# Kernel tuning notes

Hardware: AMD Instinct MI355X
Metric: run time of the kernel (lower is better)

## Reference

```python
import jax, jax.numpy as jnp
import numpy as np

UNITS = 1024
D_MODEL = 1024
H = 16
DK = 64
DV = 64
M = 128
B = 4
S = 1024


def setup_inputs() -> dict:
    key = jax.random.key(0)
    ks = jax.random.split(key, 12)
    s = 1.0 / np.sqrt(D_MODEL)
    inp = {
        "queries": jax.random.normal(ks[0], (B, S, D_MODEL), jnp.float32),
        "keys": jax.random.normal(ks[1], (B, S, D_MODEL), jnp.float32),
        "values": jax.random.normal(ks[2], (B, S, D_MODEL), jnp.float32),
        "Wq": jax.random.normal(ks[3], (D_MODEL, H * DK), jnp.float32) * s,
        "bq": jnp.zeros((H * DK,), jnp.float32),
        "Wk": jax.random.normal(ks[4], (D_MODEL, H * DK), jnp.float32) * s,
        "bk": jnp.zeros((H * DK,), jnp.float32),
        "Wv": jax.random.normal(ks[5], (D_MODEL, H * DV), jnp.float32) * s,
        "bv": jnp.zeros((H * DV,), jnp.float32),
        "Wo": jax.random.normal(ks[6], (H * DV, UNITS), jnp.float32) * (1.0 / np.sqrt(H * DV)),
        "bo": jnp.zeros((UNITS,), jnp.float32),
        "mk": jax.random.normal(ks[7], (1, M, H * DK), jnp.float32) * 0.1,
        "mv": jax.random.normal(ks[8], (1, M, H * DV), jnp.float32) * 0.1,
        "h": H,
    }
    return inp


def reference(queries, keys, values, Wq, bq, Wk, bk, Wv, bv, Wo, bo, mk, mv, h):
    Bq, Sq, _ = queries.shape
    m = mk.shape[1]
    dk = Wk.shape[1] // h
    dv = Wv.shape[1] // h
    scale_m = jnp.sqrt(jnp.asarray(m, queries.dtype))

    # Q projection: [B, h, Sq, dk]
    q = (queries @ Wq + bq).reshape(Bq, Sq, h, dk).transpose(0, 2, 1, 3)

    # K/V projections with m learned memory slots concatenated on the seq axis
    k_flat = jnp.concatenate(
        [keys @ Wk + bk, scale_m * jnp.broadcast_to(mk, (Bq, m, h * dk))], axis=1
    )  # [B, Sk+m, h*dk]
    v_flat = jnp.concatenate(
        [values @ Wv + bv, scale_m * jnp.broadcast_to(mv, (Bq, m, h * dv))], axis=1
    )  # [B, Sk+m, h*dv]
    Skm = k_flat.shape[1]
    k = k_flat.reshape(Bq, Skm, h, dk).transpose(0, 2, 1, 3)  # [B, h, Sk+m, dk]
    v = v_flat.reshape(Bq, Skm, h, dv).transpose(0, 2, 1, 3)  # [B, h, Sk+m, dv]

    # Scaled dot-product attention over sequence + memory slots
    scores = jnp.einsum("bhqd,bhkd->bhqk", q, k) / jnp.sqrt(jnp.asarray(dk, q.dtype))
    attn = jax.nn.softmax(scores, axis=-1)  # [B, h, Sq, Sk+m]
    out = jnp.einsum("bhqk,bhkd->bhqd", attn, v)  # [B, h, Sq, dv]
    out = out.transpose(0, 2, 1, 3).reshape(Bq, Sq, h * dv)
    return out @ Wo + bo
```

## Files before the change

### kernel.cpp

```cpp
#include <hip/hip_runtime.h>

typedef __attribute__((ext_vector_type(8))) __bf16 bf16x8;
typedef __attribute__((ext_vector_type(4))) float f32x4;

#define DEVINL __device__ __forceinline__

constexpr int BZ = 4;
constexpr int SEQ = 1024;
constexpr int DMODEL = 1024;
constexpr int NH = 16;
constexpr int HD = 64;
constexpr int MSLOT = 128;
constexpr int NT = BZ * SEQ;
constexpr int SKM = SEQ + MSLOT;
constexpr int VT_LD = BZ * SKM;
constexpr float SCALE_M = 11.313708498984761f;
constexpr float SCEXP = 0.18033688011112042f;
constexpr size_t OF_QIN  = 0;
constexpr size_t OF_KIN  = OF_QIN  + (size_t)NT * DMODEL;
constexpr size_t OF_VIN  = OF_KIN  + (size_t)NT * DMODEL;
constexpr size_t OF_WQT  = OF_VIN  + (size_t)NT * DMODEL;
constexpr size_t OF_WKT  = OF_WQT  + (size_t)DMODEL * DMODEL;
constexpr size_t OF_WVT  = OF_WKT  + (size_t)DMODEL * DMODEL;
constexpr size_t OF_WOT  = OF_WVT  + (size_t)DMODEL * DMODEL;
constexpr size_t OF_QB   = OF_WOT  + (size_t)DMODEL * DMODEL;
constexpr size_t OF_KPR  = OF_QB   + (size_t)NT * DMODEL;
constexpr size_t OF_KMEM = OF_KPR  + (size_t)NT * DMODEL;
constexpr size_t OF_VTG  = OF_KMEM + (size_t)MSLOT * DMODEL;
constexpr size_t OF_AOUT = OF_VTG  + (size_t)DMODEL * VT_LD;

DEVINL unsigned short f2bf(float f) {
  union { float f; unsigned u; } v; v.f = f;
  unsigned r = v.u + 0x7FFF + ((v.u >> 16) & 1);
  return (unsigned short)(r >> 16);
}

#if __has_builtin(__builtin_amdgcn_cvt_pk_bf16_f32)
DEVINL unsigned pack2(float a, float b) {
  auto t = __builtin_amdgcn_cvt_pk_bf16_f32(a, b);
  unsigned r; __builtin_memcpy(&r, &t, 4); return r;
}
#else
DEVINL unsigned pack2(float a, float b) {
  return (unsigned)f2bf(a) | ((unsigned)f2bf(b) << 16);
}
#endif

#if __has_builtin(__builtin_amdgcn_exp2f)
DEVINL float fast_exp2(float x) { return __builtin_amdgcn_exp2f(x); }
#else
DEVINL float fast_exp2(float x) { return exp2f(x); }
#endif

DEVINL f32x4 mfma16(bf16x8 a, bf16x8 b, f32x4 c) {
  return __builtin_amdgcn_mfma_f32_16x16x32_bf16(a, b, c, 0, 0, 0);
}

DEVINL void gload16(const unsigned short* gp, unsigned short* lp) {
  __builtin_amdgcn_global_load_lds(
      (const __attribute__((address_space(1))) unsigned int*)(const void*)gp,
      (__attribute__((address_space(3))) unsigned int*)(void*)lp, 16, 0, 0);
}


__global__ __launch_bounds__(256) void cvt3_bf16(const float* __restrict__ q,
                                                 const float* __restrict__ k,
                                                 const float* __restrict__ v,
                                                 unsigned short* __restrict__ dq,
                                                 unsigned short* __restrict__ dk,
                                                 unsigned short* __restrict__ dv) {
  const float* src = (blockIdx.y == 0) ? q : (blockIdx.y == 1) ? k : v;
  unsigned short* dst = (blockIdx.y == 0) ? dq : (blockIdx.y == 1) ? dk : dv;
  int i = (blockIdx.x * 256 + threadIdx.x) * 8;
  float4 v0 = *(const float4*)(src + i);
  float4 v1 = *(const float4*)(src + i + 4);
  union { unsigned u2[4]; uint4 v; } o;
  o.u2[0] = pack2(v0.x, v0.y); o.u2[1] = pack2(v0.z, v0.w);
  o.u2[2] = pack2(v1.x, v1.y); o.u2[3] = pack2(v1.z, v1.w);
  *(uint4*)(dst + i) = o.v;
}

__global__ __launch_bounds__(256) void transpose_cvt4(
    const float* __restrict__ s0, const float* __restrict__ s1,
    const float* __restrict__ s2, const float* __restrict__ s3,
    unsigned short* __restrict__ d0, unsigned short* __restrict__ d1,
    unsigned short* __restrict__ d2, unsigned short* __restrict__ d3) {
  const float* src = (blockIdx.z == 0) ? s0 : (blockIdx.z == 1) ? s1 : (blockIdx.z == 2) ? s2 : s3;
  unsigned short* dst = (blockIdx.z == 0) ? d0 : (blockIdx.z == 1) ? d1 : (blockIdx.z == 2) ? d2 : d3;
  __shared__ float t[32][65];
  const int tid = threadIdx.x;
  const int n0 = blockIdx.x * 32, k0 = blockIdx.y * 64;
  {
    int c = tid & 31, rg = tid >> 5;
#pragma unroll
    for (int rr = 0; rr < 8; ++rr)
      t[c][rg * 8 + rr] = src[(size_t)(k0 + rg * 8 + rr) * DMODEL + n0 + c];
  }
  __syncthreads();
  {
    int n = tid >> 3, ck = tid & 7;
    union { unsigned short u[8]; uint4 v; } o;
#pragma unroll
    for (int j = 0; j < 8; ++j) o.u[j] = f2bf(t[n][ck * 8 + j]);
    *(uint4*)(dst + (size_t)(n0 + n) * DMODEL + k0 + ck * 8) = o.v;
  }
}

__global__ __launch_bounds__(256) void kmem_cvt(const float* __restrict__ mk,
                                                unsigned short* __restrict__ dst) {
  int i = blockIdx.x * 256 + threadIdx.x;
  dst[i] = f2bf(mk[i] * SCALE_M);
}

__global__ __launch_bounds__(256) void vmem_transpose(const float* __restrict__ mv,
                                                      unsigned short* __restrict__ VtG) {
  __shared__ float t[32][33];
  const int tx = threadIdx.x, ty = threadIdx.y;
  const int j0 = blockIdx.x * 32, c0 = blockIdx.y * 32;
#pragma unroll
  for (int r = 0; r < 4; ++r)
    t[ty + r * 8][tx] = mv[(size_t)(j0 + ty + r * 8) * DMODEL + c0 + tx];
  __syncthreads();
#pragma unroll
  for (int r = 0; r < 4; ++r) {
    int c = c0 + ty + r * 8;
    unsigned short v = f2bf(t[tx][ty + r * 8] * SCALE_M);
#pragma unroll
    for (int bb = 0; bb < BZ; ++bb)
      VtG[(size_t)c * VT_LD + bb * SKM + SEQ + j0 + tx] = v;
  }
}


DEVINL void gemm_stage(const unsigned short* big, const unsigned short* sm,
                       unsigned short* B0, unsigned short* B1,
                       unsigned short* S0, unsigned short* S1,
                       int k0, int tid) {
#pragma unroll
  for (int hb = 0; hb < 2; ++hb) {
    unsigned short* bl = hb ? B1 : B0;
#pragma unroll
    for (int gi = 0; gi < 2; ++gi) {
      int g = gi * 256 + tid;
      int row = g >> 2, slot = g & 3;
      gload16(big + (size_t)row * DMODEL + k0 + hb * 32 + slot * 8, bl + g * 8);
    }
    unsigned short* sl = hb ? S1 : S0;
    int row = tid >> 2, slot = tid & 3;
    gload16(sm + (size_t)row * DMODEL + k0 + hb * 32 + slot * 8, sl + tid * 8);
  }
}

DEVINL void gemm_compute(const unsigned short* B0, const unsigned short* B1,
                         const unsigned short* S0, const unsigned short* S1,
                         int wr, int wc, int quad, int l16, f32x4 acc[4][2]) {
#pragma unroll
  for (int hb = 0; hb < 2; ++hb) {
    const unsigned short* bl = hb ? B1 : B0;
    const unsigned short* sl = hb ? S1 : S0;
    bf16x8 af[4], bfr[2];
#pragma unroll
    for (int rb = 0; rb < 4; ++rb)
      af[rb] = *(const bf16x8*)(bl + (wr * 64 + rb * 16 + l16) * 32 + quad * 8);
#pragma unroll
    for (int cb = 0; cb < 2; ++cb)
      bfr[cb] = *(const bf16x8*)(sl + (wc * 32 + cb * 16 + l16) * 32 + quad * 8);
#pragma unroll
    for (int rb = 0; rb < 4; ++rb)
#pragma unroll
      for (int cb = 0; cb < 2; ++cb)
        acc[rb][cb] = mfma16(af[rb], bfr[cb], acc[rb][cb]);
  }
}

__global__ __launch_bounds__(256) void proj_qkv(
    const unsigned short* __restrict__ Qin, const unsigned short* __restrict__ Kin,
    const unsigned short* __restrict__ Vin, const unsigned short* __restrict__ Wqt,
    const unsigned short* __restrict__ Wkt, const unsigned short* __restrict__ Wvt,
    const float* __restrict__ bq, const float* __restrict__ bk,
    const float* __restrict__ bv, unsigned short* __restrict__ Qbp,
    unsigned short* __restrict__ Kprp, unsigned short* __restrict__ VtG) {
  __shared__ unsigned short Big0[128 * 32], Big1[128 * 32];
  __shared__ unsigned short Sm0[64 * 32], Sm1[64 * 32];
  const int tid = threadIdx.x;
  const int pid = blockIdx.x >> 9;
  const int idx = blockIdx.x & 511;
  const int w = tid >> 6, lane = tid & 63, quad = lane >> 4, l16 = lane & 15;
  const int wr = w >> 1, wc = w & 1;
  f32x4 acc[4][2] = {};

  if (pid < 2) {
    const unsigned short* A  = pid ? Kin : Qin;
    const unsigned short* Wt = pid ? Wkt : Wqt;
    const float* bias        = pid ? bk : bq;
    unsigned short* out      = pid ? Kprp : Qbp;
    const int n0 = (idx & 15) * 64, m0 = (idx >> 4) * 128;
    const unsigned short* big = A + (size_t)m0 * DMODEL;
    const unsigned short* sm  = Wt + (size_t)n0 * DMODEL;
    for (int kt = 0; kt < 16; ++kt) {
      gemm_stage(big, sm, Big0, Big1, Sm0, Sm1, kt * 64, tid);
      __syncthreads();
      gemm_compute(Big0, Big1, Sm0, Sm1, wr, wc, quad, l16, acc);
      __syncthreads();
    }
#pragma unroll
    for (int rb = 0; rb < 4; ++rb)
#pragma unroll
      for (int cb = 0; cb < 2; ++cb)
#pragma unroll
        for (int r = 0; r < 4; ++r) {
          int row = m0 + wr * 64 + rb * 16 + quad * 4 + r;
          int col = n0 + wc * 32 + cb * 16 + l16;
          out[(size_t)row * DMODEL + col] = f2bf(acc[rb][cb][r] + bias[col]);
        }
  } else {
    const int t0 = (idx & 63) * 64, n0 = (idx >> 6) * 128;
    const unsigned short* big = Wvt + (size_t)n0 * DMODEL;
    const unsigned short* sm  = Vin + (size_t)t0 * DMODEL;
    for (int kt = 0; kt < 16; ++kt) {
      gemm_stage(big, sm, Big0, Big1, Sm0, Sm1, kt * 64, tid);
      __syncthreads();
      gemm_compute(Big0, Big1, Sm0, Sm1, wr, wc, quad, l16, acc);
      __syncthreads();
    }
#pragma unroll
    for (int rb = 0; rb < 4; ++rb)
#pragma unroll
      for (int cb = 0; cb < 2; ++cb)
#pragma unroll
        for (int r = 0; r < 4; ++r) {
          int n = n0 + wr * 64 + rb * 16 + quad * 4 + r;
          int tok = t0 + wc * 32 + cb * 16 + l16;
          int col = tok + (tok >> 10) * MSLOT;
          VtG[(size_t)n * VT_LD + col] = f2bf(acc[rb][cb][r] + bv[n]);
        }
  }
}

__global__ __launch_bounds__(256) void gemm_out(const unsigned short* __restrict__ A,
                                                const unsigned short* __restrict__ Wt,
                                                const float* __restrict__ bias,
                                                float* __restrict__ Cout) {
  __shared__ unsigned short Big0[128 * 32], Big1[128 * 32];
  __shared__ unsigned short Sm0[64 * 32], Sm1[64 * 32];
  const int tid = threadIdx.x;
  const int m0 = blockIdx.y * 128, n0 = blockIdx.x * 64;
  const int w = tid >> 6, lane = tid & 63, quad = lane >> 4, l16 = lane & 15;
  const int wr = w >> 1, wc = w & 1;
  f32x4 acc[4][2] = {};
  const unsigned short* big = A + (size_t)m0 * DMODEL;
  const unsigned short* sm  = Wt + (size_t)n0 * DMODEL;
  for (int kt = 0; kt < 16; ++kt) {
    gemm_stage(big, sm, Big0, Big1, Sm0, Sm1, kt * 64, tid);
    __syncthreads();
    gemm_compute(Big0, Big1, Sm0, Sm1, wr, wc, quad, l16, acc);
    __syncthreads();
  }
#pragma unroll
  for (int rb = 0; rb < 4; ++rb)
#pragma unroll
    for (int cb = 0; cb < 2; ++cb)
#pragma unroll
      for (int r = 0; r < 4; ++r) {
        int row = m0 + wr * 64 + rb * 16 + quad * 4 + r;
        int col = n0 + wc * 32 + cb * 16 + l16;
        Cout[(size_t)row * DMODEL + col] = acc[rb][cb][r] + bias[col];
      }
}

__global__ __launch_bounds__(256) void attn_kernel(const unsigned short* __restrict__ Qb,
                                                   const unsigned short* __restrict__ Kproj,
                                                   const unsigned short* __restrict__ Kmem,
                                                   const unsigned short* __restrict__ VtG,
                                                   unsigned short* __restrict__ Aout) {
  __shared__ unsigned short Ks[64 * 72];
  __shared__ unsigned short Vs[64 * 72];
  __shared__ unsigned short Pl[4 * 16 * 72];
  const int tid = threadIdx.x;
  const int bh = blockIdx.x & 63, qb = blockIdx.x >> 6;
  const int b = bh & 3, h = bh >> 2;
  const int w = tid >> 6, lane = tid & 63, quad = lane >> 4, l16 = lane & 15;
  const int token0 = b * SEQ + qb * 64 + w * 16;
  unsigned short* Pw = Pl + w * 16 * 72;

  const int g0 = tid, g1 = tid + 256;
  const int row0 = g0 >> 3, slot0 = g0 & 7;
  const int row1 = g1 >> 3, slot1 = g1 & 7;

  auto kbase = [&](int tile) -> const unsigned short* {
    return (tile < 16) ? Kproj + (size_t)(b * SEQ + tile * 64) * DMODEL + h * HD
                       : Kmem + (size_t)((tile - 16) * 64) * DMODEL + h * HD;
  };
  auto vbase = [&](int tile) -> const unsigned short* {
    int c0 = (tile < 16) ? b * SKM + tile * 64 : b * SKM + SEQ + (tile - 16) * 64;
    return VtG + (size_t)(h * HD) * VT_LD + c0;
  };

  bf16x8 qf[2];
#pragma unroll
  for (int t = 0; t < 2; ++t)
    qf[t] = *(const bf16x8*)(Qb + (size_t)(token0 + l16) * DMODEL + h * HD + t * 32 + quad * 8);

  f32x4 O[4] = {};
  float lsum = 0.0f;

  uint4 kr0, kr1, vr0, vr1;
  {
    const unsigned short* kp = kbase(0);
    const unsigned short* vp = vbase(0);
    kr0 = *(const uint4*)(kp + (size_t)row0 * DMODEL + slot0 * 8);
    kr1 = *(const uint4*)(kp + (size_t)row1 * DMODEL + slot1 * 8);
    vr0 = *(const uint4*)(vp + (size_t)row0 * VT_LD + slot0 * 8);
    vr1 = *(const uint4*)(vp + (size_t)row1 * VT_LD + slot1 * 8);
  }

  for (int tile = 0; tile < 18; ++tile) {
    *(uint4*)(Ks + row0 * 72 + slot0 * 8) = kr0;
    *(uint4*)(Ks + row1 * 72 + slot1 * 8) = kr1;
    *(uint4*)(Vs + row0 * 72 + slot0 * 8) = vr0;
    *(uint4*)(Vs + row1 * 72 + slot1 * 8) = vr1;
    __syncthreads();
    if (tile < 17) {
      const unsigned short* kp = kbase(tile + 1);
      const unsigned short* vp = vbase(tile + 1);
      kr0 = *(const uint4*)(kp + (size_t)row0 * DMODEL + slot0 * 8);
      kr1 = *(const uint4*)(kp + (size_t)row1 * DMODEL + slot1 * 8);
      vr0 = *(const uint4*)(vp + (size_t)row0 * VT_LD + slot0 * 8);
      vr1 = *(const uint4*)(vp + (size_t)row1 * VT_LD + slot1 * 8);
    }

    f32x4 sc[4] = {};
#pragma unroll
    for (int c = 0; c < 4; ++c)
#pragma unroll
      for (int t = 0; t < 2; ++t) {
        bf16x8 kb = *(const bf16x8*)(Ks + (c * 16 + l16) * 72 + t * 32 + quad * 8);
        sc[c] = mfma16(kb, qf[t], sc[c]);
      }

#pragma unroll
    for (int c = 0; c < 4; ++c) {
      float p0 = fast_exp2(sc[c][0] * SCEXP);
      float p1 = fast_exp2(sc[c][1] * SCEXP);
      float p2 = fast_exp2(sc[c][2] * SCEXP);
      float p3 = fast_exp2(sc[c][3] * SCEXP);
      lsum += (p0 + p1) + (p2 + p3);
      union { unsigned u[2]; } pk;
      pk.u[0] = pack2(p0, p1);
      pk.u[1] = pack2(p2, p3);
      *(uint2*)(Pw + l16 * 72 + c * 16 + quad * 4) = *(uint2*)pk.u;
    }
    __builtin_amdgcn_wave_barrier();

#pragma unroll
    for (int t2 = 0; t2 < 2; ++t2) {
      bf16x8 pa = *(const bf16x8*)(Pw + l16 * 72 + t2 * 32 + quad * 8);
#pragma unroll
      for (int c2 = 0; c2 < 4; ++c2) {
        bf16x8 vb = *(const bf16x8*)(Vs + (c2 * 16 + l16) * 72 + t2 * 32 + quad * 8);
        O[c2] = mfma16(pa, vb, O[c2]);
      }
    }
    __syncthreads();
  }

  lsum += __shfl_xor(lsum, 16);
  lsum += __shfl_xor(lsum, 32);
#pragma unroll
  for (int r = 0; r < 4; ++r) {
    float lv = __shfl(lsum, quad * 4 + r, 16);
    float inv = 1.0f / lv;
#pragma unroll
    for (int c2 = 0; c2 < 4; ++c2)
      Aout[(size_t)(token0 + quad * 4 + r) * DMODEL + h * HD + c2 * 16 + l16] =
          f2bf(O[c2][r] * inv);
  }
}

extern "C" void kernel_launch(void* const* d_in, const int* in_sizes, int n_in,
                              void* d_out, int out_size, void* d_ws, size_t ws_size,
                              hipStream_t stream) {
  const float* queries = (const float*)d_in[0];
  const float* keys    = (const float*)d_in[1];
  const float* values  = (const float*)d_in[2];
  const float* Wq = (const float*)d_in[3];
  const float* bq = (const float*)d_in[4];
  const float* Wk = (const float*)d_in[5];
  const float* bk = (const float*)d_in[6];
  const float* Wv = (const float*)d_in[7];
  const float* bv = (const float*)d_in[8];
  const float* Wo = (const float*)d_in[9];
  const float* bo = (const float*)d_in[10];
  const float* mk = (const float*)d_in[11];
  const float* mv = (const float*)d_in[12];

  unsigned short* ws = (unsigned short*)d_ws;
  unsigned short* Qin  = ws + OF_QIN;
  unsigned short* Kin  = ws + OF_KIN;
  unsigned short* Vin  = ws + OF_VIN;
  unsigned short* Wqt  = ws + OF_WQT;
  unsigned short* Wkt  = ws + OF_WKT;
  unsigned short* Wvt  = ws + OF_WVT;
  unsigned short* Wot  = ws + OF_WOT;
  unsigned short* Qbp  = ws + OF_QB;
  unsigned short* Kprp = ws + OF_KPR;
  unsigned short* Kmm  = ws + OF_KMEM;
  unsigned short* VtGp = ws + OF_VTG;
  unsigned short* Aoutp = ws + OF_AOUT;

  cvt3_bf16<<<dim3(2048, 3), 256, 0, stream>>>(queries, keys, values, Qin, Kin, Vin);

  transpose_cvt4<<<dim3(32, 16, 4), 256, 0, stream>>>(Wq, Wk, Wv, Wo, Wqt, Wkt, Wvt, Wot);

  kmem_cvt<<<(MSLOT * DMODEL) / 256, 256, 0, stream>>>(mk, Kmm);
  vmem_transpose<<<dim3(MSLOT / 32, DMODEL / 32), dim3(32, 8), 0, stream>>>(mv, VtGp);

  proj_qkv<<<1536, 256, 0, stream>>>(Qin, Kin, Vin, Wqt, Wkt, Wvt, bq, bk, bv,
                                     Qbp, Kprp, VtGp);

  attn_kernel<<<1024, 256, 0, stream>>>(Qbp, Kprp, Kmm, VtGp, Aoutp);

  gemm_out<<<dim3(16, 32), 256, 0, stream>>>(Aoutp, Wot, bo, (float*)d_out);
}
```

Measured before the change: 228.9 us.

## Enlarge GEMM tiles to 128x128 and process 32 queries per wave in attention

The projection and output GEMMs move from 128x64 tiles with a 64-wide k step to 128x128 tiles with a 32-wide k step. Each wave now holds a 4x4 accumulator block, so every loaded tile feeds more MFMAs and global traffic per FLOP drops. The attention kernel has each wave handle two 16-query groups, so each staged K/V tile in shared memory is reused for 128 queries per block. The launch grids are halved to match. The trade-offs are higher register use, fewer blocks to fill the CUs, and twice as many k-loop barriers in the GEMMs.

```diff
diff --git a/kernel.cpp b/kernel.cpp
--- a/kernel.cpp
+++ b/kernel.cpp
@@ -132,45 +132,31 @@
 }
 
 
-DEVINL void gemm_stage(const unsigned short* big, const unsigned short* sm,
-                       unsigned short* B0, unsigned short* B1,
-                       unsigned short* S0, unsigned short* S1,
-                       int k0, int tid) {
-#pragma unroll
-  for (int hb = 0; hb < 2; ++hb) {
-    unsigned short* bl = hb ? B1 : B0;
-#pragma unroll
-    for (int gi = 0; gi < 2; ++gi) {
-      int g = gi * 256 + tid;
-      int row = g >> 2, slot = g & 3;
-      gload16(big + (size_t)row * DMODEL + k0 + hb * 32 + slot * 8, bl + g * 8);
-    }
-    unsigned short* sl = hb ? S1 : S0;
-    int row = tid >> 2, slot = tid & 3;
-    gload16(sm + (size_t)row * DMODEL + k0 + hb * 32 + slot * 8, sl + tid * 8);
-  }
-}
-
-DEVINL void gemm_compute(const unsigned short* B0, const unsigned short* B1,
-                         const unsigned short* S0, const unsigned short* S1,
-                         int wr, int wc, int quad, int l16, f32x4 acc[4][2]) {
-#pragma unroll
-  for (int hb = 0; hb < 2; ++hb) {
-    const unsigned short* bl = hb ? B1 : B0;
-    const unsigned short* sl = hb ? S1 : S0;
-    bf16x8 af[4], bfr[2];
-#pragma unroll
-    for (int rb = 0; rb < 4; ++rb)
-      af[rb] = *(const bf16x8*)(bl + (wr * 64 + rb * 16 + l16) * 32 + quad * 8);
-#pragma unroll
-    for (int cb = 0; cb < 2; ++cb)
-      bfr[cb] = *(const bf16x8*)(sl + (wc * 32 + cb * 16 + l16) * 32 + quad * 8);
-#pragma unroll
-    for (int rb = 0; rb < 4; ++rb)
-#pragma unroll
-      for (int cb = 0; cb < 2; ++cb)
-        acc[rb][cb] = mfma16(af[rb], bfr[cb], acc[rb][cb]);
-  }
+DEVINL void g128_stage(const unsigned short* rA, const unsigned short* cB,
+                       unsigned short* As, unsigned short* Bs, int k0, int tid) {
+#pragma unroll
+  for (int gi = 0; gi < 2; ++gi) {
+    int g = gi * 256 + tid;
+    int row = g >> 2, slot = g & 3;
+    gload16(rA + (size_t)row * DMODEL + k0 + slot * 8, As + g * 8);
+    gload16(cB + (size_t)row * DMODEL + k0 + slot * 8, Bs + g * 8);
+  }
+}
+
+DEVINL void g128_compute(const unsigned short* As, const unsigned short* Bs,
+                         int wr, int wc, int quad, int l16, f32x4 acc[4][4]) {
+  bf16x8 af[4], bfr[4];
+#pragma unroll
+  for (int rb = 0; rb < 4; ++rb)
+    af[rb] = *(const bf16x8*)(As + (wr * 64 + rb * 16 + l16) * 32 + quad * 8);
+#pragma unroll
+  for (int cb = 0; cb < 4; ++cb)
+    bfr[cb] = *(const bf16x8*)(Bs + (wc * 64 + cb * 16 + l16) * 32 + quad * 8);
+#pragma unroll
+  for (int rb = 0; rb < 4; ++rb)
+#pragma unroll
+    for (int cb = 0; cb < 4; ++cb)
+      acc[rb][cb] = mfma16(af[rb], bfr[cb], acc[rb][cb]);
 }
 
 __global__ __launch_bounds__(256) void proj_qkv(
@@ -180,57 +166,58 @@
     const float* __restrict__ bq, const float* __restrict__ bk,
     const float* __restrict__ bv, unsigned short* __restrict__ Qbp,
     unsigned short* __restrict__ Kprp, unsigned short* __restrict__ VtG) {
-  __shared__ unsigned short Big0[128 * 32], Big1[128 * 32];
-  __shared__ unsigned short Sm0[64 * 32], Sm1[64 * 32];
+  __shared__ unsigned short As[128 * 32];
+  __shared__ unsigned short Bs[128 * 32];
   const int tid = threadIdx.x;
-  const int pid = blockIdx.x >> 9;
-  const int idx = blockIdx.x & 511;
+  const int pid = blockIdx.x >> 8;
+  const int idx = blockIdx.x & 255;
   const int w = tid >> 6, lane = tid & 63, quad = lane >> 4, l16 = lane & 15;
   const int wr = w >> 1, wc = w & 1;
-  f32x4 acc[4][2] = {};
+
+  const unsigned short *rA, *cB;
+  int m0, n0;
+  if (pid == 0) {
+    m0 = (idx >> 3) * 128; n0 = (idx & 7) * 128;
+    rA = Qin + (size_t)m0 * DMODEL; cB = Wqt + (size_t)n0 * DMODEL;
+  } else if (pid == 1) {
+    m0 = (idx >> 3) * 128; n0 = (idx & 7) * 128;
+    rA = Kin + (size_t)m0 * DMODEL; cB = Wkt + (size_t)n0 * DMODEL;
+  } else {
+    m0 = (idx & 7) * 128;
+    n0 = (idx >> 3) * 128;
+    rA = Wvt + (size_t)m0 * DMODEL; cB = Vin + (size_t)n0 * DMODEL;
+  }
+
+  f32x4 acc[4][4] = {};
+  for (int kt = 0; kt < 32; ++kt) {
+    g128_stage(rA, cB, As, Bs, kt * 32, tid);
+    __syncthreads();
+    g128_compute(As, Bs, wr, wc, quad, l16, acc);
+    __syncthreads();
+  }
 
   if (pid < 2) {
-    const unsigned short* A  = pid ? Kin : Qin;
-    const unsigned short* Wt = pid ? Wkt : Wqt;
-    const float* bias        = pid ? bk : bq;
-    unsigned short* out      = pid ? Kprp : Qbp;
-    const int n0 = (idx & 15) * 64, m0 = (idx >> 4) * 128;
-    const unsigned short* big = A + (size_t)m0 * DMODEL;
-    const unsigned short* sm  = Wt + (size_t)n0 * DMODEL;
-    for (int kt = 0; kt < 16; ++kt) {
-      gemm_stage(big, sm, Big0, Big1, Sm0, Sm1, kt * 64, tid);
-      __syncthreads();
-      gemm_compute(Big0, Big1, Sm0, Sm1, wr, wc, quad, l16, acc);
-      __syncthreads();
-    }
+    const float* bias = pid ? bk : bq;
+    unsigned short* out = pid ? Kprp : Qbp;
 #pragma unroll
     for (int rb = 0; rb < 4; ++rb)
 #pragma unroll
-      for (int cb = 0; cb < 2; ++cb)
+      for (int cb = 0; cb < 4; ++cb)
 #pragma unroll
         for (int r = 0; r < 4; ++r) {
           int row = m0 + wr * 64 + rb * 16 + quad * 4 + r;
-          int col = n0 + wc * 32 + cb * 16 + l16;
+          int col = n0 + wc * 64 + cb * 16 + l16;
           out[(size_t)row * DMODEL + col] = f2bf(acc[rb][cb][r] + bias[col]);
         }
   } else {
-    const int t0 = (idx & 63) * 64, n0 = (idx >> 6) * 128;
-    const unsigned short* big = Wvt + (size_t)n0 * DMODEL;
-    const unsigned short* sm  = Vin + (size_t)t0 * DMODEL;
-    for (int kt = 0; kt < 16; ++kt) {
-      gemm_stage(big, sm, Big0, Big1, Sm0, Sm1, kt * 64, tid);
-      __syncthreads();
-      gemm_compute(Big0, Big1, Sm0, Sm1, wr, wc, quad, l16, acc);
-      __syncthreads();
-    }
 #pragma unroll
     for (int rb = 0; rb < 4; ++rb)
 #pragma unroll
-      for (int cb = 0; cb < 2; ++cb)
+      for (int cb = 0; cb < 4; ++cb)
 #pragma unroll
         for (int r = 0; r < 4; ++r) {
-          int n = n0 + wr * 64 + rb * 16 + quad * 4 + r;
-          int tok = t0 + wc * 32 + cb * 16 + l16;
+          int n = m0 + wr * 64 + rb * 16 + quad * 4 + r;
+          int tok = n0 + wc * 64 + cb * 16 + l16;
           int col = tok + (tok >> 10) * MSLOT;
           VtG[(size_t)n * VT_LD + col] = f2bf(acc[rb][cb][r] + bv[n]);
         }
@@ -241,29 +228,29 @@
                                                 const unsigned short* __restrict__ Wt,
                                                 const float* __restrict__ bias,
                                                 float* __restrict__ Cout) {
-  __shared__ unsigned short Big0[128 * 32], Big1[128 * 32];
-  __shared__ unsigned short Sm0[64 * 32], Sm1[64 * 32];
+  __shared__ unsigned short As[128 * 32];
+  __shared__ unsigned short Bs[128 * 32];
   const int tid = threadIdx.x;
-  const int m0 = blockIdx.y * 128, n0 = blockIdx.x * 64;
+  const int m0 = blockIdx.y * 128, n0 = blockIdx.x * 128;
   const int w = tid >> 6, lane = tid & 63, quad = lane >> 4, l16 = lane & 15;
   const int wr = w >> 1, wc = w & 1;
-  f32x4 acc[4][2] = {};
-  const unsigned short* big = A + (size_t)m0 * DMODEL;
-  const unsigned short* sm  = Wt + (size_t)n0 * DMODEL;
-  for (int kt = 0; kt < 16; ++kt) {
-    gemm_stage(big, sm, Big0, Big1, Sm0, Sm1, kt * 64, tid);
-    __syncthreads();
-    gemm_compute(Big0, Big1, Sm0, Sm1, wr, wc, quad, l16, acc);
+  const unsigned short* rA = A + (size_t)m0 * DMODEL;
+  const unsigned short* cB = Wt + (size_t)n0 * DMODEL;
+  f32x4 acc[4][4] = {};
+  for (int kt = 0; kt < 32; ++kt) {
+    g128_stage(rA, cB, As, Bs, kt * 32, tid);
+    __syncthreads();
+    g128_compute(As, Bs, wr, wc, quad, l16, acc);
     __syncthreads();
   }
 #pragma unroll
   for (int rb = 0; rb < 4; ++rb)
 #pragma unroll
-    for (int cb = 0; cb < 2; ++cb)
+    for (int cb = 0; cb < 4; ++cb)
 #pragma unroll
       for (int r = 0; r < 4; ++r) {
         int row = m0 + wr * 64 + rb * 16 + quad * 4 + r;
-        int col = n0 + wc * 32 + cb * 16 + l16;
+        int col = n0 + wc * 64 + cb * 16 + l16;
         Cout[(size_t)row * DMODEL + col] = acc[rb][cb][r] + bias[col];
       }
 }
@@ -275,16 +262,16 @@
                                                    unsigned short* __restrict__ Aout) {
   __shared__ unsigned short Ks[64 * 72];
   __shared__ unsigned short Vs[64 * 72];
-  __shared__ unsigned short Pl[4 * 16 * 72];
+  __shared__ unsigned short Pl[4 * 32 * 72];
   const int tid = threadIdx.x;
   const int bh = blockIdx.x & 63, qb = blockIdx.x >> 6;
   const int b = bh & 3, h = bh >> 2;
   const int w = tid >> 6, lane = tid & 63, quad = lane >> 4, l16 = lane & 15;
-  const int token0 = b * SEQ + qb * 64 + w * 16;
-  unsigned short* Pw = Pl + w * 16 * 72;
-
-  const int g0 = tid, g1 = tid + 256;
-  const int row0 = g0 >> 3, slot0 = g0 & 7;
+  const int token0 = b * SEQ + qb * 128 + w * 32;
+  unsigned short* Pw = Pl + w * 32 * 72;
+
+  const int row0 = tid >> 3, slot0 = tid & 7;
+  const int g1 = tid + 256;
   const int row1 = g1 >> 3, slot1 = g1 & 7;
 
   auto kbase = [&](int tile) -> const unsigned short* {
@@ -296,13 +283,16 @@
     return VtG + (size_t)(h * HD) * VT_LD + c0;
   };
 
-  bf16x8 qf[2];
-#pragma unroll
-  for (int t = 0; t < 2; ++t)
-    qf[t] = *(const bf16x8*)(Qb + (size_t)(token0 + l16) * DMODEL + h * HD + t * 32 + quad * 8);
-
-  f32x4 O[4] = {};
-  float lsum = 0.0f;
+  bf16x8 qf[2][2];
+#pragma unroll
+  for (int g = 0; g < 2; ++g)
+#pragma unroll
+    for (int t = 0; t < 2; ++t)
+      qf[g][t] = *(const bf16x8*)(Qb + (size_t)(token0 + g * 16 + l16) * DMODEL +
+                                  h * HD + t * 32 + quad * 8);
+
+  f32x4 O[2][4] = {};
+  float lsum[2] = {0.0f, 0.0f};
 
   uint4 kr0, kr1, vr0, vr1;
   {
@@ -329,51 +319,59 @@
       vr1 = *(const uint4*)(vp + (size_t)row1 * VT_LD + slot1 * 8);
     }
 
-    f32x4 sc[4] = {};
-#pragma unroll
-    for (int c = 0; c < 4; ++c)
-#pragma unroll
-      for (int t = 0; t < 2; ++t) {
-        bf16x8 kb = *(const bf16x8*)(Ks + (c * 16 + l16) * 72 + t * 32 + quad * 8);
-        sc[c] = mfma16(kb, qf[t], sc[c]);
+#pragma unroll
+    for (int g = 0; g < 2; ++g) {
+      f32x4 sc[4] = {};
+#pragma unroll
+      for (int c = 0; c < 4; ++c)
+#pragma unroll
+        for (int t = 0; t < 2; ++t) {
+          bf16x8 kb = *(const bf16x8*)(Ks + (c * 16 + l16) * 72 + t * 32 + quad * 8);
+          sc[c] = mfma16(kb, qf[g][t], sc[c]);
+        }
+#pragma unroll
+      for (int c = 0; c < 4; ++c) {
+        float p0 = fast_exp2(sc[c][0] * SCEXP);
+        float p1 = fast_exp2(sc[c][1] * SCEXP);
+        float p2 = fast_exp2(sc[c][2] * SCEXP);
+        float p3 = fast_exp2(sc[c][3] * SCEXP);
+        lsum[g] += (p0 + p1) + (p2 + p3);
+        union { unsigned u[2]; } pk;
+        pk.u[0] = pack2(p0, p1);
+        pk.u[1] = pack2(p2, p3);
+        *(uint2*)(Pw + (g * 16 + l16) * 72 + c * 16 + quad * 4) = *(uint2*)pk.u;
       }
-
-#pragma unroll
-    for (int c = 0; c < 4; ++c) {
-      float p0 = fast_exp2(sc[c][0] * SCEXP);
-      float p1 = fast_exp2(sc[c][1] * SCEXP);
-      float p2 = fast_exp2(sc[c][2] * SCEXP);
-      float p3 = fast_exp2(sc[c][3] * SCEXP);
-      lsum += (p0 + p1) + (p2 + p3);
-      union { unsigned u[2]; } pk;
-      pk.u[0] = pack2(p0, p1);
-      pk.u[1] = pack2(p2, p3);
-      *(uint2*)(Pw + l16 * 72 + c * 16 + quad * 4) = *(uint2*)pk.u;
     }
     __builtin_amdgcn_wave_barrier();
 
 #pragma unroll
     for (int t2 = 0; t2 < 2; ++t2) {
-      bf16x8 pa = *(const bf16x8*)(Pw + l16 * 72 + t2 * 32 + quad * 8);
+      bf16x8 pa0 = *(const bf16x8*)(Pw + (0 + l16) * 72 + t2 * 32 + quad * 8);
+      bf16x8 pa1 = *(const bf16x8*)(Pw + (16 + l16) * 72 + t2 * 32 + quad * 8);
 #pragma unroll
       for (int c2 = 0; c2 < 4; ++c2) {
         bf16x8 vb = *(const bf16x8*)(Vs + (c2 * 16 + l16) * 72 + t2 * 32 + quad * 8);
-        O[c2] = mfma16(pa, vb, O[c2]);
+        O[0][c2] = mfma16(pa0, vb, O[0][c2]);
+        O[1][c2] = mfma16(pa1, vb, O[1][c2]);
       }
     }
     __syncthreads();
   }
 
-  lsum += __shfl_xor(lsum, 16);
-  lsum += __shfl_xor(lsum, 32);
-#pragma unroll
-  for (int r = 0; r < 4; ++r) {
-    float lv = __shfl(lsum, quad * 4 + r, 16);
-    float inv = 1.0f / lv;
-#pragma unroll
-    for (int c2 = 0; c2 < 4; ++c2)
-      Aout[(size_t)(token0 + quad * 4 + r) * DMODEL + h * HD + c2 * 16 + l16] =
-          f2bf(O[c2][r] * inv);
+#pragma unroll
+  for (int g = 0; g < 2; ++g) {
+    float ls = lsum[g];
+    ls += __shfl_xor(ls, 16);
+    ls += __shfl_xor(ls, 32);
+#pragma unroll
+    for (int r = 0; r < 4; ++r) {
+      float lv = __shfl(ls, quad * 4 + r, 16);
+      float inv = 1.0f / lv;
+#pragma unroll
+      for (int c2 = 0; c2 < 4; ++c2)
+        Aout[(size_t)(token0 + g * 16 + quad * 4 + r) * DMODEL + h * HD + c2 * 16 + l16] =
+            f2bf(O[g][c2][r] * inv);
+    }
   }
 }
 
@@ -415,10 +413,10 @@
   kmem_cvt<<<(MSLOT * DMODEL) / 256, 256, 0, stream>>>(mk, Kmm);
   vmem_transpose<<<dim3(MSLOT / 32, DMODEL / 32), dim3(32, 8), 0, stream>>>(mv, VtGp);
 
-  proj_qkv<<<1536, 256, 0, stream>>>(Qin, Kin, Vin, Wqt, Wkt, Wvt, bq, bk, bv,
-                                     Qbp, Kprp, VtGp);
-
-  attn_kernel<<<1024, 256, 0, stream>>>(Qbp, Kprp, Kmm, VtGp, Aoutp);
-
-  gemm_out<<<dim3(16, 32), 256, 0, stream>>>(Aoutp, Wot, bo, (float*)d_out);
-}
+  proj_qkv<<<768, 256, 0, stream>>>(Qin, Kin, Vin, Wqt, Wkt, Wvt, bq, bk, bv,
+                                    Qbp, Kprp, VtGp);
+
+  attn_kernel<<<512, 256, 0, stream>>>(Qbp, Kprp, Kmm, VtGp, Aoutp);
+
+  gemm_out<<<dim3(8, 32), 256, 0, stream>>>(Aoutp, Wot, bo, (float*)d_out);
+}
```

Result: slower. 245.7 us (+7.4%).

## Double query rows per attention wave and simplify output GEMM staging

Applied to the files above, without the earlier changes.

Each attention wave now handles 32 query rows instead of 16, reusing every staged K/V tile for twice the work and halving the K/V global traffic per query. The grid becomes (8,16,4), so there are half as many blocks. The output GEMM drops its shared gemm_stage/gemm_compute helpers for an inline single-buffer loop with a K-step of 32, using direct gload16 into shared memory. This trades fewer attention blocks and more registers per wave for better reuse, and the GEMM change alters how loads overlap with compute.

```diff
diff --git a/kernel.cpp b/kernel.cpp
--- a/kernel.cpp
+++ b/kernel.cpp
@@ -241,19 +241,39 @@
                                                 const unsigned short* __restrict__ Wt,
                                                 const float* __restrict__ bias,
                                                 float* __restrict__ Cout) {
-  __shared__ unsigned short Big0[128 * 32], Big1[128 * 32];
-  __shared__ unsigned short Sm0[64 * 32], Sm1[64 * 32];
+  __shared__ unsigned short As[128 * 32];
+  __shared__ unsigned short Bs[64 * 32];
   const int tid = threadIdx.x;
-  const int m0 = blockIdx.y * 128, n0 = blockIdx.x * 64;
+  const int m0 = blockIdx.y * 128;
+  const int n0 = blockIdx.x * 64;
   const int w = tid >> 6, lane = tid & 63, quad = lane >> 4, l16 = lane & 15;
   const int wr = w >> 1, wc = w & 1;
   f32x4 acc[4][2] = {};
-  const unsigned short* big = A + (size_t)m0 * DMODEL;
-  const unsigned short* sm  = Wt + (size_t)n0 * DMODEL;
-  for (int kt = 0; kt < 16; ++kt) {
-    gemm_stage(big, sm, Big0, Big1, Sm0, Sm1, kt * 64, tid);
+  for (int kt = 0; kt < 32; ++kt) {
+    const int k0 = kt * 32;
+#pragma unroll
+    for (int gi = 0; gi < 2; ++gi) {
+      int g = gi * 256 + tid;
+      int row = g >> 2, slot = g & 3;
+      gload16(A + (size_t)(m0 + row) * DMODEL + k0 + slot * 8, As + g * 8);
+    }
+    {
+      int row = tid >> 2, slot = tid & 3;
+      gload16(Wt + (size_t)(n0 + row) * DMODEL + k0 + slot * 8, Bs + tid * 8);
+    }
     __syncthreads();
-    gemm_compute(Big0, Big1, Sm0, Sm1, wr, wc, quad, l16, acc);
+    bf16x8 af[4], bfr[2];
+#pragma unroll
+    for (int rb = 0; rb < 4; ++rb)
+      af[rb] = *(const bf16x8*)(As + (wr * 64 + rb * 16 + l16) * 32 + quad * 8);
+#pragma unroll
+    for (int cb = 0; cb < 2; ++cb)
+      bfr[cb] = *(const bf16x8*)(Bs + (wc * 32 + cb * 16 + l16) * 32 + quad * 8);
+#pragma unroll
+    for (int rb = 0; rb < 4; ++rb)
+#pragma unroll
+      for (int cb = 0; cb < 2; ++cb)
+        acc[rb][cb] = mfma16(af[rb], bfr[cb], acc[rb][cb]);
     __syncthreads();
   }
 #pragma unroll
@@ -275,16 +295,15 @@
                                                    unsigned short* __restrict__ Aout) {
   __shared__ unsigned short Ks[64 * 72];
   __shared__ unsigned short Vs[64 * 72];
-  __shared__ unsigned short Pl[4 * 16 * 72];
+  __shared__ unsigned short Pl[4 * 32 * 72];
   const int tid = threadIdx.x;
-  const int bh = blockIdx.x & 63, qb = blockIdx.x >> 6;
-  const int b = bh & 3, h = bh >> 2;
+  const int qb = blockIdx.x, h = blockIdx.y, b = blockIdx.z;
   const int w = tid >> 6, lane = tid & 63, quad = lane >> 4, l16 = lane & 15;
-  const int token0 = b * SEQ + qb * 64 + w * 16;
-  unsigned short* Pw = Pl + w * 16 * 72;
-
-  const int g0 = tid, g1 = tid + 256;
-  const int row0 = g0 >> 3, slot0 = g0 & 7;
+  const int token0 = b * SEQ + qb * 128 + w * 32;
+  unsigned short* Pw = Pl + w * 32 * 72;
+
+  const int row0 = tid >> 3, slot0 = tid & 7;
+  const int g1 = tid + 256;
   const int row1 = g1 >> 3, slot1 = g1 & 7;
 
   auto kbase = [&](int tile) -> const unsigned short* {
@@ -296,13 +315,16 @@
     return VtG + (size_t)(h * HD) * VT_LD + c0;
   };
 
-  bf16x8 qf[2];
-#pragma unroll
-  for (int t = 0; t < 2; ++t)
-    qf[t] = *(const bf16x8*)(Qb + (size_t)(token0 + l16) * DMODEL + h * HD + t * 32 + quad * 8);
-
-  f32x4 O[4] = {};
-  float lsum = 0.0f;
+  bf16x8 qf[2][2];
+#pragma unroll
+  for (int g = 0; g < 2; ++g)
+#pragma unroll
+    for (int t = 0; t < 2; ++t)
+      qf[g][t] = *(const bf16x8*)(Qb + (size_t)(token0 + g * 16 + l16) * DMODEL +
+                                  h * HD + t * 32 + quad * 8);
+
+  f32x4 O[2][4] = {};
+  float lsum[2] = {0.0f, 0.0f};
 
   uint4 kr0, kr1, vr0, vr1;
   {
@@ -329,51 +351,59 @@
       vr1 = *(const uint4*)(vp + (size_t)row1 * VT_LD + slot1 * 8);
     }
 
-    f32x4 sc[4] = {};
-#pragma unroll
-    for (int c = 0; c < 4; ++c)
-#pragma unroll
-      for (int t = 0; t < 2; ++t) {
-        bf16x8 kb = *(const bf16x8*)(Ks + (c * 16 + l16) * 72 + t * 32 + quad * 8);
-        sc[c] = mfma16(kb, qf[t], sc[c]);
+#pragma unroll
+    for (int g = 0; g < 2; ++g) {
+      f32x4 sc[4] = {};
+#pragma unroll
+      for (int c = 0; c < 4; ++c)
+#pragma unroll
+        for (int t = 0; t < 2; ++t) {
+          bf16x8 kb = *(const bf16x8*)(Ks + (c * 16 + l16) * 72 + t * 32 + quad * 8);
+          sc[c] = mfma16(kb, qf[g][t], sc[c]);
+        }
+#pragma unroll
+      for (int c = 0; c < 4; ++c) {
+        float p0 = fast_exp2(sc[c][0] * SCEXP);
+        float p1 = fast_exp2(sc[c][1] * SCEXP);
+        float p2 = fast_exp2(sc[c][2] * SCEXP);
+        float p3 = fast_exp2(sc[c][3] * SCEXP);
+        lsum[g] += (p0 + p1) + (p2 + p3);
+        union { unsigned u[2]; } pk;
+        pk.u[0] = pack2(p0, p1);
+        pk.u[1] = pack2(p2, p3);
+        *(uint2*)(Pw + (g * 16 + l16) * 72 + c * 16 + quad * 4) = *(uint2*)pk.u;
       }
-
-#pragma unroll
-    for (int c = 0; c < 4; ++c) {
-      float p0 = fast_exp2(sc[c][0] * SCEXP);
-      float p1 = fast_exp2(sc[c][1] * SCEXP);
-      float p2 = fast_exp2(sc[c][2] * SCEXP);
-      float p3 = fast_exp2(sc[c][3] * SCEXP);
-      lsum += (p0 + p1) + (p2 + p3);
-      union { unsigned u[2]; } pk;
-      pk.u[0] = pack2(p0, p1);
-      pk.u[1] = pack2(p2, p3);
-      *(uint2*)(Pw + l16 * 72 + c * 16 + quad * 4) = *(uint2*)pk.u;
     }
     __builtin_amdgcn_wave_barrier();
 
 #pragma unroll
     for (int t2 = 0; t2 < 2; ++t2) {
-      bf16x8 pa = *(const bf16x8*)(Pw + l16 * 72 + t2 * 32 + quad * 8);
+      bf16x8 pa0 = *(const bf16x8*)(Pw + (0 + l16) * 72 + t2 * 32 + quad * 8);
+      bf16x8 pa1 = *(const bf16x8*)(Pw + (16 + l16) * 72 + t2 * 32 + quad * 8);
 #pragma unroll
       for (int c2 = 0; c2 < 4; ++c2) {
         bf16x8 vb = *(const bf16x8*)(Vs + (c2 * 16 + l16) * 72 + t2 * 32 + quad * 8);
-        O[c2] = mfma16(pa, vb, O[c2]);
+        O[0][c2] = mfma16(pa0, vb, O[0][c2]);
+        O[1][c2] = mfma16(pa1, vb, O[1][c2]);
       }
     }
     __syncthreads();
   }
 
-  lsum += __shfl_xor(lsum, 16);
-  lsum += __shfl_xor(lsum, 32);
-#pragma unroll
-  for (int r = 0; r < 4; ++r) {
-    float lv = __shfl(lsum, quad * 4 + r, 16);
-    float inv = 1.0f / lv;
-#pragma unroll
-    for (int c2 = 0; c2 < 4; ++c2)
-      Aout[(size_t)(token0 + quad * 4 + r) * DMODEL + h * HD + c2 * 16 + l16] =
-          f2bf(O[c2][r] * inv);
+#pragma unroll
+  for (int g = 0; g < 2; ++g) {
+    float ls = lsum[g];
+    ls += __shfl_xor(ls, 16);
+    ls += __shfl_xor(ls, 32);
+#pragma unroll
+    for (int r = 0; r < 4; ++r) {
+      float lv = __shfl(ls, quad * 4 + r, 16);
+      float inv = 1.0f / lv;
+#pragma unroll
+      for (int c2 = 0; c2 < 4; ++c2)
+        Aout[(size_t)(token0 + g * 16 + quad * 4 + r) * DMODEL + h * HD + c2 * 16 + l16] =
+            f2bf(O[g][c2][r] * inv);
+    }
   }
 }
 
@@ -418,7 +448,7 @@
   proj_qkv<<<1536, 256, 0, stream>>>(Qin, Kin, Vin, Wqt, Wkt, Wvt, bq, bk, bv,
                                      Qbp, Kprp, VtGp);
 
-  attn_kernel<<<1024, 256, 0, stream>>>(Qbp, Kprp, Kmm, VtGp, Aoutp);
+  attn_kernel<<<dim3(8, 16, 4), 256, 0, stream>>>(Qbp, Kprp, Kmm, VtGp, Aoutp);
 
   gemm_out<<<dim3(16, 32), 256, 0, stream>>>(Aoutp, Wot, bo, (float*)d_out);
 }
```

Result: no change. 231.9 us (+1.3%).
